# Optimization experiments

Hardware: AMD Instinct MI355X
Metric: run time of the kernel (lower is better)

Reference implementation:

```python
import jax, jax.numpy as jnp
import numpy as np

S = 4096
T_STEPS = 2048

def setup_inputs() -> dict:
    key = jax.random.key(0)
    k1, k2, k3 = jax.random.split(key, 3)
    # initial log-prior over S states
    log_M0 = jax.nn.log_softmax(jax.random.normal(k1, (S,), dtype=jnp.float32))
    # transition log-probs: log_trans[i, j] = log p(x_t = i | x_{t-1} = j)
    # (logsumexp in the torch code is over dim=1 = previous state, so columns normalize)
    log_trans = jax.nn.log_softmax(jax.random.normal(k2, (S, S), dtype=jnp.float32), axis=0)
    # per-step emission log-likelihoods log f_t(y_t | x_t), t = 0..T
    log_emit = 0.5 * jax.random.normal(k3, (T_STEPS + 1, S), dtype=jnp.float32)
    return {"log_M0": log_M0, "log_trans": log_trans, "log_emit": log_emit, "T": T_STEPS}

def reference(log_M0, log_trans, log_emit, T):
    # initialise(): unnormalized filter at t=0
    unnorm0 = log_M0 + log_emit[0]                       # [S]
    lf0 = jax.nn.logsumexp(unnorm0)                      # scalar log-normalizer
    filt0 = unnorm0 - lf0

    def step(carry, emit_t):
        filt, lik = carry
        # prediction_i = logsumexp_j( filter_j + log_trans[i, j] )
        pred = jax.nn.logsumexp(filt[None, :] + log_trans, axis=1)   # [S]
        unnorm = pred + emit_t                                        # [S]
        lf = jax.nn.logsumexp(unnorm)
        return (unnorm - lf, lik + lf), None

    (_, likelihood), _ = jax.lax.scan(step, (filt0, lf0), log_emit[1:T + 1])
    # forward() returns the accumulated sum of per-step likelihood factors = total log-likelihood
    return likelihood
```

## Files before the change

kernel.cpp:

```cpp
#include <hip/hip_runtime.h>
#include <hip/hip_bf16.h>

#define SS 4096
#define TT 2048

typedef float v4f __attribute__((ext_vector_type(4)));


__device__ __forceinline__ void llc_load4x4(const v4f* p,
                                            v4f& a, v4f& b, v4f& c, v4f& d) {
  asm volatile(
      "global_load_dwordx4 %0, %4, off sc0 sc1\n\t"
      "global_load_dwordx4 %1, %5, off sc0 sc1\n\t"
      "global_load_dwordx4 %2, %6, off sc0 sc1\n\t"
      "global_load_dwordx4 %3, %7, off sc0 sc1\n\t"
      "s_waitcnt vmcnt(0)"
      : "=&v"(a), "=&v"(b), "=&v"(c), "=&v"(d)
      : "v"(p), "v"(p + 256), "v"(p + 512), "v"(p + 768)
      : "memory");
}

__device__ __forceinline__ void llc_store4_drain(v4f* p, v4f v) {
  asm volatile("global_store_dwordx4 %0, %1, off sc0 sc1\n\t"
               "s_waitcnt vmcnt(0)"
               :: "v"(p), "v"(v) : "memory");
}


__device__ __forceinline__ unsigned short f2bf_rn(float f) {
  unsigned int u = __float_as_uint(f);
  u += 0x7FFFu + ((u >> 16) & 1u);
  return (unsigned short)(u >> 16);
}

__device__ __forceinline__ unsigned orsgn(v4f v, unsigned e) {
  return (__float_as_uint(v.x) ^ e) | (__float_as_uint(v.y) ^ e)
       | (__float_as_uint(v.z) ^ e) | (__float_as_uint(v.w) ^ e);
}

__device__ __forceinline__ uint4 xorsgn(v4f v, unsigned e) {
  uint4 r;
  r.x = __float_as_uint(v.x) ^ e;  r.y = __float_as_uint(v.y) ^ e;
  r.z = __float_as_uint(v.z) ^ e;  r.w = __float_as_uint(v.w) ^ e;
  return r;
}

__device__ __forceinline__ float dot8(uint4 u, v4f qa, v4f qb, float acc) {
  acc = fmaf(__uint_as_float(u.x << 16),          qa.x, acc);
  acc = fmaf(__uint_as_float(u.x & 0xFFFF0000u),  qa.y, acc);
  acc = fmaf(__uint_as_float(u.y << 16),          qa.z, acc);
  acc = fmaf(__uint_as_float(u.y & 0xFFFF0000u),  qa.w, acc);
  acc = fmaf(__uint_as_float(u.z << 16),          qb.x, acc);
  acc = fmaf(__uint_as_float(u.z & 0xFFFF0000u),  qb.y, acc);
  acc = fmaf(__uint_as_float(u.w << 16),          qb.z, acc);
  acc = fmaf(__uint_as_float(u.w & 0xFFFF0000u),  qb.w, acc);
  return acc;
}

__global__ void prep_E(const float* __restrict__ lt, unsigned short* __restrict__ E) {
  size_t base = ((size_t)blockIdx.x * 256 + threadIdx.x) * 8;
  float4 a = ((const float4*)(lt + base))[0];
  float4 b = ((const float4*)(lt + base))[1];
  uint4 o;
  o.x = (unsigned)f2bf_rn(__expf(a.x)) | ((unsigned)f2bf_rn(__expf(a.y)) << 16);
  o.y = (unsigned)f2bf_rn(__expf(a.z)) | ((unsigned)f2bf_rn(__expf(a.w)) << 16);
  o.z = (unsigned)f2bf_rn(__expf(b.x)) | ((unsigned)f2bf_rn(__expf(b.y)) << 16);
  o.w = (unsigned)f2bf_rn(__expf(b.z)) | ((unsigned)f2bf_rn(__expf(b.w)) << 16);
  ((uint4*)(E + base))[0] = o;
}

__global__ void init_q(const float* __restrict__ m0, const float* __restrict__ emit,
                       float* __restrict__ q) {
  int i = blockIdx.x * 256 + threadIdx.x;
  q[i] = __expf(m0[i] + emit[i]);
}

__global__ void __launch_bounds__(256, 1)
hmm_fwd(const unsigned short* __restrict__ E, const float* __restrict__ emit,
        float* q, float* out) {
  __shared__ unsigned short es[16 * SS];
  __shared__ float qs[SS];
  __shared__ float wsum[4];
  const int b    = blockIdx.x;
  const int tid  = threadIdx.x;
  const int wave = tid >> 6;
  const int lane = tid & 63;
  const int row0 = (b << 4) + (wave << 2);

  {
    const uint4* src = (const uint4*)(E + ((size_t)b << 4) * SS);
    uint4* dst = (uint4*)es;
#pragma unroll
    for (int i = 0; i < 32; ++i)
      dst[tid + (i << 8)] = src[tid + (i << 8)];
  }
  __syncthreads();

  const uint4* ev = (const uint4*)es;
  const uint4* e0 = ev + (size_t)((wave << 2) + 0) * 512;
  const uint4* e1 = ev + (size_t)((wave << 2) + 1) * 512;
  const uint4* e2 = ev + (size_t)((wave << 2) + 2) * 512;
  const uint4* e3 = ev + (size_t)((wave << 2) + 3) * 512;

  for (int t = 1; t <= TT; ++t) {
    const unsigned e = (unsigned)(((t - 1) >> 1) & 1) << 31;
    {
      const v4f* qsrc4 = (const v4f*)(q + ((t - 1) & 1) * SS);
      v4f va, vb, vc, vd;
      for (;;) {
        llc_load4x4(qsrc4 + tid, va, vb, vc, vd);
        unsigned o = orsgn(va, e) | orsgn(vb, e) | orsgn(vc, e) | orsgn(vd, e);
        if (!(o >> 31)) break;
      }
      uint4* qs4 = (uint4*)qs;
      qs4[tid]       = xorsgn(va, e);
      qs4[tid + 256] = xorsgn(vb, e);
      qs4[tid + 512] = xorsgn(vc, e);
      qs4[tid + 768] = xorsgn(vd, e);
    }
    __syncthreads();

    v4f em;
    if (lane == 0) em = *(const v4f*)(emit + (size_t)t * SS + row0);

    float acc0 = 0.f, acc1 = 0.f, acc2 = 0.f, acc3 = 0.f;
#pragma unroll
    for (int k = 0; k < 8; ++k) {
      int vi = (k << 6) + lane;
      const v4f* qp = (const v4f*)(qs + (k << 9) + (lane << 3));
      v4f qa = qp[0], qb = qp[1];
      acc0 = dot8(e0[vi], qa, qb, acc0);
      acc1 = dot8(e1[vi], qa, qb, acc1);
      acc2 = dot8(e2[vi], qa, qb, acc2);
      acc3 = dot8(e3[vi], qa, qb, acc3);
    }
#pragma unroll
    for (int m = 32; m > 0; m >>= 1) {
      acc0 += __shfl_xor(acc0, m);
      acc1 += __shfl_xor(acc1, m);
      acc2 += __shfl_xor(acc2, m);
      acc3 += __shfl_xor(acc3, m);
    }

    float* qdst = q + (t & 1) * SS;
    if (lane == 0) {
      float scale = ((t & 255) == 0) ? 0x1p-46f : 1.0f;
      if ((t >> 1) & 1) scale = -scale;
      v4f r;
      r.x = acc0 * (__expf(em.x) * scale);
      r.y = acc1 * (__expf(em.y) * scale);
      r.z = acc2 * (__expf(em.z) * scale);
      r.w = acc3 * (__expf(em.w) * scale);
      llc_store4_drain((v4f*)(qdst + row0), r);
    }
    __syncthreads();
  }

  if (b == 0) {
    const v4f* qf4 = (const v4f*)q;
    v4f va, vb, vc, vd;
    for (;;) {
      llc_load4x4(qf4 + tid, va, vb, vc, vd);
      unsigned o = orsgn(va, 0) | orsgn(vb, 0) | orsgn(vc, 0) | orsgn(vd, 0);
      if (!(o >> 31)) break;
    }
    float s = va.x + va.y + va.z + va.w + vb.x + vb.y + vb.z + vb.w
            + vc.x + vc.y + vc.z + vc.w + vd.x + vd.y + vd.z + vd.w;
#pragma unroll
    for (int m = 32; m > 0; m >>= 1) s += __shfl_xor(s, m);
    if (lane == 0) wsum[wave] = s;
    __syncthreads();
    if (tid == 0) {
      float tot = wsum[0] + wsum[1] + wsum[2] + wsum[3];
      out[0] = logf(tot) + 368.0f * 0.693147180559945f;
    }
  }
}

extern "C" void kernel_launch(void* const* d_in, const int* in_sizes, int n_in,
                              void* d_out, int out_size, void* d_ws, size_t ws_size,
                              hipStream_t stream) {
  const float* log_M0    = (const float*)d_in[0];
  const float* log_trans = (const float*)d_in[1];
  const float* log_emit  = (const float*)d_in[2];

  unsigned short* E = (unsigned short*)d_ws;
  float* q  = (float*)((char*)d_ws + (size_t)SS * SS * 2);
  float* out = (float*)d_out;

  hipLaunchKernelGGL(prep_E, dim3((SS * SS) / 2048), dim3(256), 0, stream, log_trans, E);
  hipLaunchKernelGGL(init_q, dim3(SS / 256), dim3(256), 0, stream, log_M0, log_emit, q);
  hipLaunchKernelGGL(hmm_fwd, dim3(256), dim3(256), 0, stream, E, log_emit, q, out);
}
```

Before: 4.998 ms.

## Keep fp32 exp transition rows in registers instead of bf16 LDS copy

Drops the separate prep kernel that converted exp(log_trans) to bf16, and has each block load its 16 rows straight from log_trans, exponentiate them, and keep them as fp32 in 256 VGPRs per thread. The per-step dot product now reads only q from LDS, with no bf16 unpacking, and the emission load is issued before the spin-wait so it overlaps with it. This removes the prep pass, the LDS traffic for the matrix and the unpack ALU work, and restores fp32 precision. The cost is very high register pressure, which risks spills, since launch bounds allow one block per CU.

```diff
diff --git a/kernel.cpp b/kernel.cpp
--- a/kernel.cpp
+++ b/kernel.cpp
@@ -1,5 +1,4 @@
 #include <hip/hip_runtime.h>
-#include <hip/hip_bf16.h>
 
 #define SS 4096
 #define TT 2048
@@ -27,12 +26,6 @@
 }
 
 
-__device__ __forceinline__ unsigned short f2bf_rn(float f) {
-  unsigned int u = __float_as_uint(f);
-  u += 0x7FFFu + ((u >> 16) & 1u);
-  return (unsigned short)(u >> 16);
-}
-
 __device__ __forceinline__ unsigned orsgn(v4f v, unsigned e) {
   return (__float_as_uint(v.x) ^ e) | (__float_as_uint(v.y) ^ e)
        | (__float_as_uint(v.z) ^ e) | (__float_as_uint(v.w) ^ e);
@@ -45,30 +38,6 @@
   return r;
 }
 
-__device__ __forceinline__ float dot8(uint4 u, v4f qa, v4f qb, float acc) {
-  acc = fmaf(__uint_as_float(u.x << 16),          qa.x, acc);
-  acc = fmaf(__uint_as_float(u.x & 0xFFFF0000u),  qa.y, acc);
-  acc = fmaf(__uint_as_float(u.y << 16),          qa.z, acc);
-  acc = fmaf(__uint_as_float(u.y & 0xFFFF0000u),  qa.w, acc);
-  acc = fmaf(__uint_as_float(u.z << 16),          qb.x, acc);
-  acc = fmaf(__uint_as_float(u.z & 0xFFFF0000u),  qb.y, acc);
-  acc = fmaf(__uint_as_float(u.w << 16),          qb.z, acc);
-  acc = fmaf(__uint_as_float(u.w & 0xFFFF0000u),  qb.w, acc);
-  return acc;
-}
-
-__global__ void prep_E(const float* __restrict__ lt, unsigned short* __restrict__ E) {
-  size_t base = ((size_t)blockIdx.x * 256 + threadIdx.x) * 8;
-  float4 a = ((const float4*)(lt + base))[0];
-  float4 b = ((const float4*)(lt + base))[1];
-  uint4 o;
-  o.x = (unsigned)f2bf_rn(__expf(a.x)) | ((unsigned)f2bf_rn(__expf(a.y)) << 16);
-  o.y = (unsigned)f2bf_rn(__expf(a.z)) | ((unsigned)f2bf_rn(__expf(a.w)) << 16);
-  o.z = (unsigned)f2bf_rn(__expf(b.x)) | ((unsigned)f2bf_rn(__expf(b.y)) << 16);
-  o.w = (unsigned)f2bf_rn(__expf(b.z)) | ((unsigned)f2bf_rn(__expf(b.w)) << 16);
-  ((uint4*)(E + base))[0] = o;
-}
-
 __global__ void init_q(const float* __restrict__ m0, const float* __restrict__ emit,
                        float* __restrict__ q) {
   int i = blockIdx.x * 256 + threadIdx.x;
@@ -76,9 +45,8 @@
 }
 
 __global__ void __launch_bounds__(256, 1)
-hmm_fwd(const unsigned short* __restrict__ E, const float* __restrict__ emit,
+hmm_fwd(const float* __restrict__ lt, const float* __restrict__ emit,
         float* q, float* out) {
-  __shared__ unsigned short es[16 * SS];
   __shared__ float qs[SS];
   __shared__ float wsum[4];
   const int b    = blockIdx.x;
@@ -87,22 +55,24 @@
   const int lane = tid & 63;
   const int row0 = (b << 4) + (wave << 2);
 
-  {
-    const uint4* src = (const uint4*)(E + ((size_t)b << 4) * SS);
-    uint4* dst = (uint4*)es;
+  v4f er[64];
 #pragma unroll
-    for (int i = 0; i < 32; ++i)
-      dst[tid + (i << 8)] = src[tid + (i << 8)];
+  for (int r = 0; r < 4; ++r) {
+    const float* src = lt + (size_t)(row0 + r) * SS + (lane << 2);
+#pragma unroll
+    for (int k = 0; k < 16; ++k) {
+      v4f v = *(const v4f*)(src + (k << 8));
+      v4f e;
+      e.x = __expf(v.x);  e.y = __expf(v.y);
+      e.z = __expf(v.z);  e.w = __expf(v.w);
+      er[r * 16 + k] = e;
+    }
   }
-  __syncthreads();
-
-  const uint4* ev = (const uint4*)es;
-  const uint4* e0 = ev + (size_t)((wave << 2) + 0) * 512;
-  const uint4* e1 = ev + (size_t)((wave << 2) + 1) * 512;
-  const uint4* e2 = ev + (size_t)((wave << 2) + 2) * 512;
-  const uint4* e3 = ev + (size_t)((wave << 2) + 3) * 512;
 
   for (int t = 1; t <= TT; ++t) {
+    v4f em;
+    if (lane == 0) em = *(const v4f*)(emit + (size_t)t * SS + row0);
+
     const unsigned e = (unsigned)(((t - 1) >> 1) & 1) << 31;
     {
       const v4f* qsrc4 = (const v4f*)(q + ((t - 1) & 1) * SS);
@@ -120,20 +90,20 @@
     }
     __syncthreads();
 
-    v4f em;
-    if (lane == 0) em = *(const v4f*)(emit + (size_t)t * SS + row0);
-
-    float acc0 = 0.f, acc1 = 0.f, acc2 = 0.f, acc3 = 0.f;
+    v4f a0 = {0.f, 0.f, 0.f, 0.f}, a1 = a0, a2 = a0, a3 = a0;
+    const v4f* qv4 = (const v4f*)qs;
 #pragma unroll
-    for (int k = 0; k < 8; ++k) {
-      int vi = (k << 6) + lane;
-      const v4f* qp = (const v4f*)(qs + (k << 9) + (lane << 3));
-      v4f qa = qp[0], qb = qp[1];
-      acc0 = dot8(e0[vi], qa, qb, acc0);
-      acc1 = dot8(e1[vi], qa, qb, acc1);
-      acc2 = dot8(e2[vi], qa, qb, acc2);
-      acc3 = dot8(e3[vi], qa, qb, acc3);
+    for (int k = 0; k < 16; ++k) {
+      v4f qv = qv4[(k << 6) + lane];
+      a0 += er[k]      * qv;
+      a1 += er[16 + k] * qv;
+      a2 += er[32 + k] * qv;
+      a3 += er[48 + k] * qv;
     }
+    float acc0 = (a0.x + a0.y) + (a0.z + a0.w);
+    float acc1 = (a1.x + a1.y) + (a1.z + a1.w);
+    float acc2 = (a2.x + a2.y) + (a2.z + a2.w);
+    float acc3 = (a3.x + a3.y) + (a3.z + a3.w);
 #pragma unroll
     for (int m = 32; m > 0; m >>= 1) {
       acc0 += __shfl_xor(acc0, m);
@@ -184,11 +154,9 @@
   const float* log_trans = (const float*)d_in[1];
   const float* log_emit  = (const float*)d_in[2];
 
-  unsigned short* E = (unsigned short*)d_ws;
-  float* q  = (float*)((char*)d_ws + (size_t)SS * SS * 2);
+  float* q   = (float*)d_ws;
   float* out = (float*)d_out;
 
-  hipLaunchKernelGGL(prep_E, dim3((SS * SS) / 2048), dim3(256), 0, stream, log_trans, E);
   hipLaunchKernelGGL(init_q, dim3(SS / 256), dim3(256), 0, stream, log_M0, log_emit, q);
-  hipLaunchKernelGGL(hmm_fwd, dim3(256), dim3(256), 0, stream, E, log_emit, q, out);
+  hipLaunchKernelGGL(hmm_fwd, dim3(256), dim3(256), 0, stream, log_trans, log_emit, q, out);
 }
```

Measured after the change: 5.244 ms. +4.9%, slower.
